# Kernel optimization log

Measured on AMD Instinct MI355X. Metric: run time of the kernel, lower is better.

Reference implementation:

```python
import jax, jax.numpy as jnp
import numpy as np

NUM_UNITS = 64
MEM_SLOTS = 8192
D_ATT = 64
D_MEM = 64
MASK_P = 0.2
NEG_INF = -1e9  # finite stand-in for RandomMask's -inf (identical softmax, safe grads)


def setup_inputs() -> dict:
    key = jax.random.key(0)
    k1, k2, k3, k4 = jax.random.split(key, 4)
    attention = jax.random.normal(k1, (NUM_UNITS, D_ATT), dtype=jnp.float32)
    attentions = jax.random.normal(k2, (NUM_UNITS, MEM_SLOTS, D_ATT), dtype=jnp.float32)
    memories = jax.random.normal(k3, (NUM_UNITS, MEM_SLOTS, D_MEM), dtype=jnp.float32)
    tmpr = jnp.ones((NUM_UNITS, 1), dtype=jnp.float32) * np.sqrt(D_ATT).astype(np.float32)
    mask = jax.random.bernoulli(k4, MASK_P, (NUM_UNITS, MEM_SLOTS))  # True -> dropped
    return {"attention": attention, "attentions": attentions,
            "memories": memories, "tmpr": tmpr, "mask": mask}


def reference(attention, attentions, memories, tmpr, mask):
    # scores: [U, M] = batched matvec over memory slots
    w = jnp.einsum('umd,ud->um', attentions, attention)
    w = jnp.where(mask, NEG_INF, w)          # RandomMask
    w = w / tmpr                              # per-unit temperature [U,1]
    weights = jax.nn.softmax(w, axis=-1)      # softmax over memory slots
    outputs = jnp.einsum('um,umd->ud', weights, memories)
    return (outputs, weights, memories)
```

## Files before the change

kernel.cpp:

```cpp
#include <hip/hip_runtime.h>
#include <cstdint>

#define U_UNITS 64
#define M_SLOTS 8192
#define D_DIM   64
#define SCH     16
#define CHUNK   (M_SLOTS / SCH)
#define BLK     256

__global__ __launch_bounds__(BLK) void fused_kernel(
    const float* __restrict__ att,
    const float* __restrict__ atts,
    const float* __restrict__ tmpr,
    const int*   __restrict__ mask,
    const float* __restrict__ mem,
    float* __restrict__ out_w,
    float* __restrict__ out_m,
    float* __restrict__ pmax,
    float* __restrict__ psum,
    float* __restrict__ pout)
{
    const int b = blockIdx.x;
    const int u = b / SCH, c = b % SCH;
    const int tid = threadIdx.x;

    __shared__ float s_att[D_DIM];
    __shared__ float s_w[CHUNK];
    __shared__ float s_m[4], s_s[4];
    __shared__ float s_acc[4 * D_DIM];

    if (tid < D_DIM) s_att[tid] = att[u * D_DIM + tid];
    __syncthreads();

    const int cg = (tid & 15) * 4;
    const float a0 = s_att[cg], a1 = s_att[cg + 1];
    const float a2 = s_att[cg + 2], a3 = s_att[cg + 3];
    const float invt = 1.0f / tmpr[u];

    const size_t ubase = (size_t)u * M_SLOTS * D_DIM + (size_t)c * CHUNK * D_DIM;
    const float* __restrict__ abase = atts + ubase;

    float lmx = -1e30f;
    #pragma unroll 4
    for (int k = 0; k < CHUNK / 16; ++k) {
        const int sl = k * 16 + (tid >> 4);
        const float4 v = *(const float4*)(abase + (size_t)sl * D_DIM + cg);
        float d = v.x * a0 + v.y * a1 + v.z * a2 + v.w * a3;
        d += __shfl_xor(d, 1);
        d += __shfl_xor(d, 2);
        d += __shfl_xor(d, 4);
        d += __shfl_xor(d, 8);
        const float wv = mask[u * M_SLOTS + c * CHUNK + sl] ? -1e30f : d * invt;
        lmx = fmaxf(lmx, wv);
        if ((tid & 15) == 0) s_w[sl] = wv;
    }
    #pragma unroll
    for (int off = 1; off < 64; off <<= 1) lmx = fmaxf(lmx, __shfl_xor(lmx, off));
    if ((tid & 63) == 0) s_m[tid >> 6] = lmx;
    __syncthreads();
    const float mx = fmaxf(fmaxf(s_m[0], s_m[1]), fmaxf(s_m[2], s_m[3]));

    const float* __restrict__ mbase = mem + ubase;
    float* __restrict__ obase = out_m + ubase;
    float acc0 = 0.f, acc1 = 0.f, acc2 = 0.f, acc3 = 0.f;
    float sm = 0.f;
    #pragma unroll 4
    for (int k = 0; k < CHUNK / 16; ++k) {
        const int sl = k * 16 + (tid >> 4);
        const float we = __expf(s_w[sl] - mx);
        const float4 v = *(const float4*)(mbase + (size_t)sl * D_DIM + cg);
        *(float4*)(obase + (size_t)sl * D_DIM + cg) = v;
        acc0 += we * v.x;
        acc1 += we * v.y;
        acc2 += we * v.z;
        acc3 += we * v.w;
        sm += we;
        if ((tid & 15) == 0)
            out_w[(size_t)u * M_SLOTS + c * CHUNK + sl] = we;
    }

    float acc[4] = {acc0, acc1, acc2, acc3};
    #pragma unroll
    for (int j = 0; j < 4; ++j) {
        acc[j] += __shfl_xor(acc[j], 16);
        acc[j] += __shfl_xor(acc[j], 32);
    }
    #pragma unroll
    for (int off = 1; off < 64; off <<= 1) sm += __shfl_xor(sm, off);

    const int lane = tid & 63, w = tid >> 6;
    if (lane == 0) s_s[w] = sm;
    if (lane < 16) {
        #pragma unroll
        for (int j = 0; j < 4; ++j) s_acc[w * D_DIM + lane * 4 + j] = acc[j];
    }
    __syncthreads();
    if (tid < D_DIM) {
        const float s = s_acc[tid] + s_acc[D_DIM + tid]
                      + s_acc[2 * D_DIM + tid] + s_acc[3 * D_DIM + tid];
        pout[(size_t)b * D_DIM + tid] = s;
    }
    if (tid == 0) {
        pmax[b] = mx;
        psum[b] = (s_s[0] + s_s[1] + s_s[2] + s_s[3]) * 0.0625f;
    }
}

__global__ void combine_out_kernel(
    const float* __restrict__ pmax,
    const float* __restrict__ psum,
    const float* __restrict__ pout,
    float* __restrict__ alpha,
    float* __restrict__ out_o)
{
    const int u = blockIdx.x, t = threadIdx.x;
    float mx = -1e30f;
    #pragma unroll
    for (int c = 0; c < SCH; ++c) mx = fmaxf(mx, pmax[u * SCH + c]);
    float s = 0.f;
    #pragma unroll
    for (int c = 0; c < SCH; ++c) s += psum[u * SCH + c] * __expf(pmax[u * SCH + c] - mx);
    const float inv = 1.0f / s;
    float o = 0.f;
    #pragma unroll
    for (int c = 0; c < SCH; ++c)
        o += __expf(pmax[u * SCH + c] - mx) * inv * pout[((size_t)u * SCH + c) * D_DIM + t];
    out_o[u * D_DIM + t] = o;
    if (t < SCH) alpha[u * SCH + t] = __expf(pmax[u * SCH + t] - mx) * inv;
}

__global__ __launch_bounds__(BLK) void wfix_kernel(
    const float* __restrict__ alpha,
    float* __restrict__ out_w)
{
    const int g = blockIdx.x * BLK + threadIdx.x;
    const int u = g >> 11;
    const int c = (g & 2047) >> 7;
    const float a = alpha[u * SCH + c];
    float4* p = reinterpret_cast<float4*>(out_w) + g;
    float4 v = *p;
    v.x *= a; v.y *= a; v.z *= a; v.w *= a;
    *p = v;
}

extern "C" void kernel_launch(void* const* d_in, const int* in_sizes, int n_in,
                              void* d_out, int out_size, void* d_ws, size_t ws_size,
                              hipStream_t stream)
{
    const float* att  = (const float*)d_in[0];
    const float* atts = (const float*)d_in[1];
    const float* mem  = (const float*)d_in[2];
    const float* tmpr = (const float*)d_in[3];
    const int*   mask = (const int*)d_in[4];

    float* out   = (float*)d_out;
    float* out_o = out;
    float* out_w = out + U_UNITS * D_DIM;
    float* out_m = out_w + (size_t)U_UNITS * M_SLOTS;

    float* ws    = (float*)d_ws;
    float* pmax  = ws;
    float* psum  = pmax + U_UNITS * SCH;
    float* alpha = psum + U_UNITS * SCH;
    float* pout  = alpha + U_UNITS * SCH;

    fused_kernel<<<U_UNITS * SCH, BLK, 0, stream>>>(
        att, atts, tmpr, mask, mem, out_w, out_m, pmax, psum, pout);
    combine_out_kernel<<<U_UNITS, D_DIM, 0, stream>>>(pmax, psum, pout, alpha, out_o);
    wfix_kernel<<<(U_UNITS * M_SLOTS / 4) / BLK, BLK, 0, stream>>>(alpha, out_w);
}
```

Before: 331.7 us.

## Fuse score and memory passes into single-pass online softmax per chunk

Merges the separate score pass and weighted-memory pass into one loop that streams attentions and memories together and keeps a running max and rescaled accumulator (online softmax). Raw scaled scores are written to out_w and normalised later in wfix using a per-unit global max and inverse sum, instead of per-chunk alpha scaling. The mask chunk is staged in shared memory, the chunk count is doubled for more blocks, and launch bounds request higher occupancy. In exchange it adds two extra exps per element in the main loop and moves exp work into the fixup kernel.

```diff
diff --git a/kernel.cpp b/kernel.cpp
--- a/kernel.cpp
+++ b/kernel.cpp
@@ -4,11 +4,11 @@
 #define U_UNITS 64
 #define M_SLOTS 8192
 #define D_DIM   64
-#define SCH     16
+#define SCH     32
 #define CHUNK   (M_SLOTS / SCH)
 #define BLK     256
 
-__global__ __launch_bounds__(BLK) void fused_kernel(
+__global__ __launch_bounds__(BLK, 8) void fused_kernel(
     const float* __restrict__ att,
     const float* __restrict__ atts,
     const float* __restrict__ tmpr,
@@ -25,74 +25,79 @@
     const int tid = threadIdx.x;
 
     __shared__ float s_att[D_DIM];
-    __shared__ float s_w[CHUNK];
+    __shared__ int   s_mask[CHUNK];
     __shared__ float s_m[4], s_s[4];
     __shared__ float s_acc[4 * D_DIM];
 
     if (tid < D_DIM) s_att[tid] = att[u * D_DIM + tid];
+    if (tid < CHUNK / 4)
+        ((int4*)s_mask)[tid] = ((const int4*)(mask + (size_t)u * M_SLOTS + c * CHUNK))[tid];
     __syncthreads();
 
-    const int cg = (tid & 15) * 4;
+    const int grp = tid >> 4;
+    const int cg  = (tid & 15) * 4;
     const float a0 = s_att[cg], a1 = s_att[cg + 1];
     const float a2 = s_att[cg + 2], a3 = s_att[cg + 3];
     const float invt = 1.0f / tmpr[u];
 
     const size_t ubase = (size_t)u * M_SLOTS * D_DIM + (size_t)c * CHUNK * D_DIM;
     const float* __restrict__ abase = atts + ubase;
+    const float* __restrict__ mbase = mem + ubase;
+    float* __restrict__ obase = out_m + ubase;
 
-    float lmx = -1e30f;
+    float m = -1e30f, sm = 0.f;
+    float acc0 = 0.f, acc1 = 0.f, acc2 = 0.f, acc3 = 0.f;
+
     #pragma unroll 4
     for (int k = 0; k < CHUNK / 16; ++k) {
-        const int sl = k * 16 + (tid >> 4);
-        const float4 v = *(const float4*)(abase + (size_t)sl * D_DIM + cg);
-        float d = v.x * a0 + v.y * a1 + v.z * a2 + v.w * a3;
+        const int sl = k * 16 + grp;
+        const float4 va = *(const float4*)(abase + (size_t)sl * D_DIM + cg);
+        const float4 vm = *(const float4*)(mbase + (size_t)sl * D_DIM + cg);
+        *(float4*)(obase + (size_t)sl * D_DIM + cg) = vm;
+
+        float d = va.x * a0 + va.y * a1 + va.z * a2 + va.w * a3;
         d += __shfl_xor(d, 1);
         d += __shfl_xor(d, 2);
         d += __shfl_xor(d, 4);
         d += __shfl_xor(d, 8);
-        const float wv = mask[u * M_SLOTS + c * CHUNK + sl] ? -1e30f : d * invt;
-        lmx = fmaxf(lmx, wv);
-        if ((tid & 15) == 0) s_w[sl] = wv;
-    }
-    #pragma unroll
-    for (int off = 1; off < 64; off <<= 1) lmx = fmaxf(lmx, __shfl_xor(lmx, off));
-    if ((tid & 63) == 0) s_m[tid >> 6] = lmx;
-    __syncthreads();
-    const float mx = fmaxf(fmaxf(s_m[0], s_m[1]), fmaxf(s_m[2], s_m[3]));
+        const float wv = s_mask[sl] ? -1e30f : d * invt;
+        if ((tid & 15) == 0)
+            out_w[(size_t)u * M_SLOTS + c * CHUNK + sl] = wv;
 
-    const float* __restrict__ mbase = mem + ubase;
-    float* __restrict__ obase = out_m + ubase;
-    float acc0 = 0.f, acc1 = 0.f, acc2 = 0.f, acc3 = 0.f;
-    float sm = 0.f;
-    #pragma unroll 4
-    for (int k = 0; k < CHUNK / 16; ++k) {
-        const int sl = k * 16 + (tid >> 4);
-        const float we = __expf(s_w[sl] - mx);
-        const float4 v = *(const float4*)(mbase + (size_t)sl * D_DIM + cg);
-        *(float4*)(obase + (size_t)sl * D_DIM + cg) = v;
-        acc0 += we * v.x;
-        acc1 += we * v.y;
-        acc2 += we * v.z;
-        acc3 += we * v.w;
-        sm += we;
-        if ((tid & 15) == 0)
-            out_w[(size_t)u * M_SLOTS + c * CHUNK + sl] = we;
+        const float newm = fmaxf(m, wv);
+        const float scf  = __expf(m - newm);
+        const float e    = __expf(wv - newm);
+        acc0 = acc0 * scf + e * vm.x;
+        acc1 = acc1 * scf + e * vm.y;
+        acc2 = acc2 * scf + e * vm.z;
+        acc3 = acc3 * scf + e * vm.w;
+        sm   = sm * scf + e;
+        m    = newm;
     }
 
-    float acc[4] = {acc0, acc1, acc2, acc3};
+    float wm = m;
+    wm = fmaxf(wm, __shfl_xor(wm, 16));
+    wm = fmaxf(wm, __shfl_xor(wm, 32));
+    const float f = __expf(m - wm);
+    float acc[4] = {acc0 * f, acc1 * f, acc2 * f, acc3 * f};
+    sm *= f;
     #pragma unroll
     for (int j = 0; j < 4; ++j) {
         acc[j] += __shfl_xor(acc[j], 16);
         acc[j] += __shfl_xor(acc[j], 32);
     }
-    #pragma unroll
-    for (int off = 1; off < 64; off <<= 1) sm += __shfl_xor(sm, off);
+    sm += __shfl_xor(sm, 16);
+    sm += __shfl_xor(sm, 32);
 
     const int lane = tid & 63, w = tid >> 6;
-    if (lane == 0) s_s[w] = sm;
+    if (lane == 0) s_m[w] = wm;
+    __syncthreads();
+    const float bmx = fmaxf(fmaxf(s_m[0], s_m[1]), fmaxf(s_m[2], s_m[3]));
+    const float f2  = __expf(wm - bmx);
+    if (lane == 0) s_s[w] = sm * f2;
     if (lane < 16) {
         #pragma unroll
-        for (int j = 0; j < 4; ++j) s_acc[w * D_DIM + lane * 4 + j] = acc[j];
+        for (int j = 0; j < 4; ++j) s_acc[w * D_DIM + lane * 4 + j] = acc[j] * f2;
     }
     __syncthreads();
     if (tid < D_DIM) {
@@ -101,8 +106,8 @@
         pout[(size_t)b * D_DIM + tid] = s;
     }
     if (tid == 0) {
-        pmax[b] = mx;
-        psum[b] = (s_s[0] + s_s[1] + s_s[2] + s_s[3]) * 0.0625f;
+        pmax[b] = bmx;
+        psum[b] = s_s[0] + s_s[1] + s_s[2] + s_s[3];
     }
 }
 
@@ -110,7 +115,8 @@
     const float* __restrict__ pmax,
     const float* __restrict__ psum,
     const float* __restrict__ pout,
-    float* __restrict__ alpha,
+    float* __restrict__ gmx,
+    float* __restrict__ ginv,
     float* __restrict__ out_o)
 {
     const int u = blockIdx.x, t = threadIdx.x;
@@ -124,22 +130,25 @@
     float o = 0.f;
     #pragma unroll
     for (int c = 0; c < SCH; ++c)
-        o += __expf(pmax[u * SCH + c] - mx) * inv * pout[((size_t)u * SCH + c) * D_DIM + t];
-    out_o[u * D_DIM + t] = o;
-    if (t < SCH) alpha[u * SCH + t] = __expf(pmax[u * SCH + t] - mx) * inv;
+        o += __expf(pmax[u * SCH + c] - mx) * pout[((size_t)u * SCH + c) * D_DIM + t];
+    out_o[u * D_DIM + t] = o * inv;
+    if (t == 0) { gmx[u] = mx; ginv[u] = inv; }
 }
 
 __global__ __launch_bounds__(BLK) void wfix_kernel(
-    const float* __restrict__ alpha,
+    const float* __restrict__ gmx,
+    const float* __restrict__ ginv,
     float* __restrict__ out_w)
 {
     const int g = blockIdx.x * BLK + threadIdx.x;
     const int u = g >> 11;
-    const int c = (g & 2047) >> 7;
-    const float a = alpha[u * SCH + c];
+    const float a = gmx[u], gi = ginv[u];
     float4* p = reinterpret_cast<float4*>(out_w) + g;
     float4 v = *p;
-    v.x *= a; v.y *= a; v.z *= a; v.w *= a;
+    v.x = __expf(v.x - a) * gi;
+    v.y = __expf(v.y - a) * gi;
+    v.z = __expf(v.z - a) * gi;
+    v.w = __expf(v.w - a) * gi;
     *p = v;
 }
 
@@ -161,11 +170,12 @@
     float* ws    = (float*)d_ws;
     float* pmax  = ws;
     float* psum  = pmax + U_UNITS * SCH;
-    float* alpha = psum + U_UNITS * SCH;
-    float* pout  = alpha + U_UNITS * SCH;
+    float* gmx   = psum + U_UNITS * SCH;
+    float* ginv  = gmx + U_UNITS;
+    float* pout  = ginv + U_UNITS;
 
     fused_kernel<<<U_UNITS * SCH, BLK, 0, stream>>>(
         att, atts, tmpr, mask, mem, out_w, out_m, pmax, psum, pout);
-    combine_out_kernel<<<U_UNITS, D_DIM, 0, stream>>>(pmax, psum, pout, alpha, out_o);
-    wfix_kernel<<<(U_UNITS * M_SLOTS / 4) / BLK, BLK, 0, stream>>>(alpha, out_w);
+    combine_out_kernel<<<U_UNITS, D_DIM, 0, stream>>>(pmax, psum, pout, gmx, ginv, out_o);
+    wfix_kernel<<<(U_UNITS * M_SLOTS / 4) / BLK, BLK, 0, stream>>>(gmx, ginv, out_w);
 }
```

Measured after the change: 336.9 us. No clear change (+1.5%).
